# Kernel optimization log

Hardware: AMD Instinct MI355X
Metric: run time of the kernel (lower is better)

The kernel has to match this reference:

```python
import jax, jax.numpy as jnp
import numpy as np

jax.config.update("jax_enable_x64", True)

MANT_SCALE = 8388608.0  # 2**23


def _decode_fp32_bits(bits):
    """[..., 32] {0,1} pulses (MSB-first IEEE-754 float32) -> float64 value."""
    f64 = jnp.float64
    sign = 1.0 - 2.0 * bits[..., 0].astype(f64)
    e = jnp.einsum('...j,j->...', bits[..., 1:9].astype(f64),
                   jnp.exp2(jnp.arange(7, -1, -1, dtype=f64)))
    frac = jnp.einsum('...j,j->...', bits[..., 9:32].astype(f64),
                      jnp.exp2(-jnp.arange(1, 24, dtype=f64)))
    normal = sign * jnp.exp2(e - 127.0) * (1.0 + frac)
    subnorm = sign * jnp.exp2(-126.0) * frac
    return jnp.where(e > 0, normal, subnorm)


def _encode_fp32_bits(y):
    """float64 value already on the fp32 grid -> [..., 32] {0,1} pulses (MSB-first)."""
    f64 = jnp.float64
    sbit = (y < 0).astype(f64)
    a = jnp.abs(y)
    e = jnp.clip(jnp.floor(jnp.log2(jnp.where(a > 0, a, 1.0))), -126.0, 127.0)
    eb = jnp.where(a > 0, e + 127.0, 0.0)          # biased exponent, 0 for zero/subnormal
    frac = jnp.where(eb > 0, a * jnp.exp2(-e) - 1.0, a * jnp.exp2(126.0))
    mant = frac * MANT_SCALE                        # exact integer for fp32-grid y
    ebits = jnp.mod(jnp.floor(eb[..., None] * jnp.exp2(-jnp.arange(7, -1, -1, dtype=f64))), 2.0)
    mbits = jnp.mod(jnp.floor(mant[..., None] * jnp.exp2(-jnp.arange(22, -1, -1, dtype=f64))), 2.0)
    bits = jnp.concatenate([sbit[..., None], ebits, mbits], axis=-1)
    return jnp.where((a > 0)[..., None], bits, 0.0).astype(jnp.float32)


def setup_inputs() -> dict:
    rng = np.random.default_rng(0)
    vals = (rng.standard_normal((1, 2048, 1024)) * 2.0).astype(np.float32)
    words = vals.view(np.uint32)
    shifts = np.arange(31, -1, -1, dtype=np.uint32)
    bits = ((words[..., None] >> shifts) & np.uint32(1)).astype(np.float32)
    return {"x": jnp.asarray(bits)}


def reference(x):
    # GELU(x) ~= x * sigmoid(1.702 * x), all intermediates in fp64 (as the
    # gate-level pipeline does), final result rounded once to fp32 bits.
    xv = _decode_fp32_bits(x)
    y64 = xv * jax.nn.sigmoid(1.702 * xv)
    y32 = y64.astype(jnp.float32).astype(jnp.float64)  # FP64 -> FP32 rounding
    return _encode_fp32_bits(y32)
```

## Files before the change

### kernel.cpp

```cpp
#include <hip/hip_runtime.h>
#include <math.h>

__global__ __launch_bounds__(256) void spike_gelu_kernel(
    const uint4* __restrict__ in, uint4* __restrict__ out, int n_vals) {
#pragma clang fp contract(off)
  const double LN2 = 0x1.62e42fefa39efp-1;

  __shared__ double Wdec[8], Vdec[23], Lm[23];
  __shared__ uint32_t lds_w[256];

  const int tid = threadIdx.x;
  if (tid < 8)       Wdec[tid]      = exp((double)(7 - tid) * LN2);
  else if (tid < 31) Vdec[tid - 8]  = exp((double)(7 - tid) * LN2);
  else if (tid < 54) Lm[tid - 31]   = exp((double)(31 - tid) * LN2);

  const int n_chunks = n_vals * 8;
  const int blk_chunk0 = blockIdx.x * 2048;

  const int nibshift = 28 - 4 * (tid & 7);
#pragma unroll
  for (int i = 0; i < 8; ++i) {
    int g = blk_chunk0 + i * 256 + tid;
    uint32_t nib = 0;
    if (g < n_chunks) {
      uint4 b = in[g];
      nib = (((b.x >> 23) & 1u) << 3) | (((b.y >> 23) & 1u) << 2) |
            (((b.z >> 23) & 1u) << 1) | ((b.w >> 23) & 1u);
    }
    uint32_t part = nib << nibshift;
    part |= __shfl_xor(part, 1);
    part |= __shfl_xor(part, 2);
    part |= __shfl_xor(part, 4);
    if ((tid & 7) == 0) lds_w[i * 32 + (tid >> 3)] = part;
  }
  __syncthreads();

  const int v = blockIdx.x * 256 + tid;
  uint32_t ob = 0;
  if (v < n_vals) {
    const uint32_t w = lds_w[tid];

    double sign = (w >> 31) ? -1.0 : 1.0;
    double e_c = 0.0;
#pragma unroll
    for (int j = 0; j < 8; ++j)
      if ((w >> (30 - j)) & 1u) e_c = e_c + Wdec[j];
    double frac_d = 0.0;
#pragma unroll
    for (int j = 0; j < 23; ++j)
      if ((w >> (22 - j)) & 1u) frac_d = frac_d + Vdec[j];

    double x;
    if (e_c > 0.0) {
      double E1 = exp((e_c - 127.0) * LN2);
      x = (sign * E1) * (1.0 + frac_d);
    } else {
      x = (sign * exp(-126.0 * LN2)) * frac_d;
    }

    double t = 1.702 * x;
    double s = 1.0 / (1.0 + exp(-t));
    double y = x * s;
    float yf = (float)y;
    double yd = (double)yf;

    double a = fabs(yd);
    if (a > 0.0) {
      if (yd < 0.0) ob |= 0x80000000u;
      double e0 = floor(log(a) / LN2);
      e0 = fmin(fmax(e0, -126.0), 127.0);
      double eb = e0 + 127.0;
      double p2 = exp(-e0 * LN2);
      double m1 = a * p2;
      double frac_e = m1 - 1.0;
      double mant = frac_e * 8388608.0;
#pragma unroll
      for (int sc = 7; sc >= 0; --sc) {
        double f = floor(eb * Lm[sc]);
        double md = f - 2.0 * floor(0.5 * f);
        ob |= ((uint32_t)md) << (23 + sc);
      }
#pragma unroll
      for (int sc = 22; sc >= 0; --sc) {
        double f = floor(mant * Lm[sc]);
        double md = f - 2.0 * floor(0.5 * f);
        ob |= ((uint32_t)md) << sc;
      }
    }
  }
  lds_w[tid] = ob;
  __syncthreads();

#pragma unroll
  for (int i = 0; i < 8; ++i) {
    int g = blk_chunk0 + i * 256 + tid;
    if (g < n_chunks) {
      uint32_t wv = lds_w[i * 32 + (tid >> 3)];
      int base = 31 - 4 * (tid & 7);
      uint4 o;
      o.x = ((wv >> base) & 1u) * 0x3F800000u;
      o.y = ((wv >> (base - 1)) & 1u) * 0x3F800000u;
      o.z = ((wv >> (base - 2)) & 1u) * 0x3F800000u;
      o.w = ((wv >> (base - 3)) & 1u) * 0x3F800000u;
      out[g] = o;
    }
  }
}

extern "C" void kernel_launch(void* const* d_in, const int* in_sizes, int n_in,
                              void* d_out, int out_size, void* d_ws, size_t ws_size,
                              hipStream_t stream) {
  int n_vals = in_sizes[0] / 32;
  const int block = 256;
  int grid = (n_vals + block - 1) / block;
  spike_gelu_kernel<<<grid, block, 0, stream>>>(
      (const uint4*)d_in[0], (uint4*)d_out, n_vals);
}
```

Before: 437.6 us.

## Precompute exponent/power tables in a setup kernel and replace per-element exp/log

```diff
diff --git a/kernel.cpp b/kernel.cpp
--- a/kernel.cpp
+++ b/kernel.cpp
@@ -1,18 +1,61 @@
 #include <hip/hip_runtime.h>
 #include <math.h>
 
+
+#define LN2C 0x1.62e42fefa39efp-1
+
+__global__ __launch_bounds__(256) void build_tables(double* __restrict__ dt,
+                                                    uint32_t* __restrict__ et) {
+#pragma clang fp contract(off)
+  const double LN2 = LN2C;
+  __shared__ double Wdec[8], Lms[23];
+  const int t = threadIdx.x;
+  if (t < 8) Wdec[t] = exp((double)(7 - t) * LN2);
+  if (t >= 31 && t < 54) Lms[t - 31] = exp((double)(31 - t) * LN2);
+  __syncthreads();
+
+  if (t == 0) {
+    dt[0] = exp(-126.0 * LN2);
+    et[0] = 0u;
+  } else {
+    double e_c = 0.0;
+#pragma unroll
+    for (int j = 0; j < 8; ++j)
+      if ((t >> (7 - j)) & 1) e_c = e_c + Wdec[j];
+    dt[t] = exp((e_c - 127.0) * LN2);
+  }
+  if (t < 23) dt[256 + t] = exp((double)(-1 - t) * LN2);
+  if (t < 23) dt[279 + t] = Lms[t];
+  if (t < 254) {
+    double e0 = (double)(t - 126);
+    dt[302 + t] = exp(-e0 * LN2);
+  }
+  if (t >= 1 && t < 255) {
+    double eb = (double)t;
+    uint32_t r = 0;
+#pragma unroll
+    for (int sc = 7; sc >= 0; --sc) {
+      double f = floor(eb * Lms[sc]);
+      double md = f - 2.0 * floor(0.5 * f);
+      r |= ((uint32_t)md) << (23 + sc);
+    }
+    et[t] = r;
+  }
+}
+
 __global__ __launch_bounds__(256) void spike_gelu_kernel(
-    const uint4* __restrict__ in, uint4* __restrict__ out, int n_vals) {
+    const uint4* __restrict__ in, uint4* __restrict__ out,
+    const double* __restrict__ dt, const uint32_t* __restrict__ et,
+    int n_vals) {
 #pragma clang fp contract(off)
-  const double LN2 = 0x1.62e42fefa39efp-1;
-
-  __shared__ double Wdec[8], Vdec[23], Lm[23];
+  const double LN2 = LN2C;
+  __shared__ double dtab[556];
+  __shared__ uint32_t etab[256];
   __shared__ uint32_t lds_w[256];
 
   const int tid = threadIdx.x;
-  if (tid < 8)       Wdec[tid]      = exp((double)(7 - tid) * LN2);
-  else if (tid < 31) Vdec[tid - 8]  = exp((double)(7 - tid) * LN2);
-  else if (tid < 54) Lm[tid - 31]   = exp((double)(31 - tid) * LN2);
+  for (int i = tid; i < 556; i += 256) dtab[i] = dt[i];
+  if (tid < 255) etab[tid] = et[tid];
 
   const int n_chunks = n_vals * 8;
   const int blk_chunk0 = blockIdx.x * 2048;
@@ -39,24 +82,21 @@
   uint32_t ob = 0;
   if (v < n_vals) {
     const uint32_t w = lds_w[tid];
+    const double* E1t  = dtab;
+    const double* Vdec = dtab + 256;
+    const double* Lm   = dtab + 279;
+    const double* P2t  = dtab + 302;
 
     double sign = (w >> 31) ? -1.0 : 1.0;
-    double e_c = 0.0;
-#pragma unroll
-    for (int j = 0; j < 8; ++j)
-      if ((w >> (30 - j)) & 1u) e_c = e_c + Wdec[j];
     double frac_d = 0.0;
 #pragma unroll
     for (int j = 0; j < 23; ++j)
       if ((w >> (22 - j)) & 1u) frac_d = frac_d + Vdec[j];
 
+    const uint32_t eidx = (w >> 23) & 0xFFu;
     double x;
-    if (e_c > 0.0) {
-      double E1 = exp((e_c - 127.0) * LN2);
-      x = (sign * E1) * (1.0 + frac_d);
-    } else {
-      x = (sign * exp(-126.0 * LN2)) * frac_d;
-    }
+    if (eidx > 0) x = (sign * E1t[eidx]) * (1.0 + frac_d);
+    else          x = (sign * E1t[0]) * frac_d;
 
     double t = 1.702 * x;
     double s = 1.0 / (1.0 + exp(-t));
@@ -67,24 +107,28 @@
     double a = fabs(yd);
     if (a > 0.0) {
       if (yd < 0.0) ob |= 0x80000000u;
-      double e0 = floor(log(a) / LN2);
-      e0 = fmin(fmax(e0, -126.0), 127.0);
-      double eb = e0 + 127.0;
-      double p2 = exp(-e0 * LN2);
+      uint32_t yb = __float_as_uint(yf);
+      uint32_t Ef = (yb >> 23) & 0xFFu;
+      uint32_t mb = yb & 0x7FFFFFu;
+      int e0i;
+      if (Ef == 0u) {
+        e0i = -126;
+      } else if (mb != 0u) {
+        e0i = (int)Ef - 127;
+      } else {
+        double e0 = floor(log(a) / LN2);
+        e0 = fmin(fmax(e0, -126.0), 127.0);
+        e0i = (int)e0;
+      }
+      double p2 = P2t[e0i + 126];
       double m1 = a * p2;
       double frac_e = m1 - 1.0;
       double mant = frac_e * 8388608.0;
-#pragma unroll
-      for (int sc = 7; sc >= 0; --sc) {
-        double f = floor(eb * Lm[sc]);
-        double md = f - 2.0 * floor(0.5 * f);
-        ob |= ((uint32_t)md) << (23 + sc);
-      }
+      ob |= etab[e0i + 127];
 #pragma unroll
       for (int sc = 22; sc >= 0; --sc) {
         double f = floor(mant * Lm[sc]);
-        double md = f - 2.0 * floor(0.5 * f);
-        ob |= ((uint32_t)md) << sc;
+        ob |= (uint32_t)(((int)f) & 1) << sc;
       }
     }
   }
@@ -111,8 +155,11 @@
                               void* d_out, int out_size, void* d_ws, size_t ws_size,
                               hipStream_t stream) {
   int n_vals = in_sizes[0] / 32;
+  double* dt = (double*)d_ws;
+  uint32_t* et = (uint32_t*)((char*)d_ws + 556 * sizeof(double));
+  build_tables<<<1, 256, 0, stream>>>(dt, et);
   const int block = 256;
   int grid = (n_vals + block - 1) / block;
   spike_gelu_kernel<<<grid, block, 0, stream>>>(
-      (const uint4*)d_in[0], (uint4*)d_out, n_vals);
+      (const uint4*)d_in[0], (uint4*)d_out, dt, et, n_vals);
 }
```

Result: no change. 432.0 us (-1.3%).
